# Optimization experiments

Measured on AMD Instinct MI355X. Metric: run time of the kernel, lower is better.

Reference implementation:

```python
import jax, jax.numpy as jnp
import numpy as np

B, N, D, E, C = 8, 4096, 1024, 512, 4096


def setup_inputs() -> dict:
    key = jax.random.key(0)
    k1, k2, k3 = jax.random.split(key, 3)
    x = jax.random.normal(k1, (B, N, D), dtype=jnp.float32)
    # xavier_normal_ scale for an (input_dim, codebook_dim) matrix
    scale = (2.0 / (D + E)) ** 0.5
    random_projection = jax.random.normal(k2, (D, E), dtype=jnp.float32) * scale
    codebook = jax.random.normal(k3, (C, E), dtype=jnp.float32)
    return {"x": x, "random_projection": random_projection, "codebook": codebook}


def _l2norm(v, eps=1e-12):
    # matches torch.nn.functional.normalize(p=2): v / max(||v||, eps)
    return v / jnp.maximum(jnp.linalg.norm(v, axis=-1, keepdims=True), eps)


def reference(x, random_projection, codebook):
    # project: b n d, d e -> b n e
    proj = jnp.einsum("bnd,de->bne", x, random_projection)
    pn = _l2norm(proj)            # [B, N, E], unit vectors
    cn = _l2norm(codebook)        # [C, E],   unit vectors
    # For unit vectors, ||p - c||^2 = 2 - 2 * <p, c>, so
    # argmin_c cdist == argmax_c cosine similarity (same indices as torch code).
    sim = jnp.einsum("bne,ce->bnc", pn, cn)  # [B, N, C]
    xq = jnp.argmax(sim, axis=-1).astype(jnp.int32)  # [B, N]
    return xq
```

## Files before the change

kernel.cpp:

```cpp
#include <hip/hip_runtime.h>
#include <math.h>


typedef _Float16 half8 __attribute__((ext_vector_type(8)));
typedef _Float16 half4 __attribute__((ext_vector_type(4)));
typedef float f32x4 __attribute__((ext_vector_type(4)));

#define INV2048 (4.8828125e-4f)
#define MARGIN 0.03f

struct Split { _Float16 h, l; };

__device__ __forceinline__ Split split_f32(float v) {
    Split s;
    s.h = (_Float16)v;
    s.l = (_Float16)((v - (float)s.h) * 2048.0f);
    return s;
}

__device__ __forceinline__ void gl_lds16(const void* g, void* l) {
    __builtin_amdgcn_global_load_lds(
        (const __attribute__((address_space(1))) unsigned int*)g,
        (__attribute__((address_space(3))) unsigned int*)l, 16, 0, 0);
}

__global__ __launch_bounds__(256) void k_prep_rpt(const float* __restrict__ rp,
                                                  _Float16* __restrict__ th,
                                                  _Float16* __restrict__ tl,
                                                  int* __restrict__ cnt) {
    if (blockIdx.x == 0 && blockIdx.y == 0 && threadIdx.x == 0) *cnt = 0;
    __shared__ float tile[64][65];
    const int k0 = blockIdx.x * 64, n0 = blockIdx.y * 64;
    const int t = threadIdx.x;
    const int rr = t >> 6, cc = t & 63;
    #pragma unroll
    for (int i = 0; i < 16; ++i) {
        int r = i * 4 + rr;
        tile[r][cc] = rp[(size_t)(k0 + r) * 512 + n0 + cc];
    }
    __syncthreads();
    #pragma unroll
    for (int i = 0; i < 16; ++i) {
        int n = i * 4 + rr;
        Split s = split_f32(tile[cc][n]);
        size_t o = (size_t)(n0 + n) * 1024 + k0 + cc;
        th[o] = s.h;
        tl[o] = s.l;
    }
}

__global__ __launch_bounds__(256) void k_norm_cb(const float* __restrict__ cb,
                                                 _Float16* __restrict__ ch,
                                                 _Float16* __restrict__ cl) {
    const int c = blockIdx.x;
    const int t = threadIdx.x;
    const float* row = cb + (size_t)c * 512;
    float v0 = row[t];
    float v1 = row[t + 256];
    float ss = v0 * v0 + v1 * v1;
    #pragma unroll
    for (int o = 32; o > 0; o >>= 1) ss += __shfl_down(ss, o, 64);
    __shared__ float wsum[4];
    if ((t & 63) == 0) wsum[t >> 6] = ss;
    __syncthreads();
    float s = 1.0f / fmaxf(sqrtf(wsum[0] + wsum[1] + wsum[2] + wsum[3]), 1e-12f);
    Split s0 = split_f32(v0 * s);
    ch[(size_t)c * 512 + t] = s0.h;
    cl[(size_t)c * 512 + t] = s0.l;
    Split s1 = split_f32(v1 * s);
    ch[(size_t)c * 512 + t + 256] = s1.h;
    cl[(size_t)c * 512 + t + 256] = s1.l;
}

__global__ __launch_bounds__(256, 2) void k_gemm1(const float* __restrict__ X,
                                                  const _Float16* __restrict__ Bh,
                                                  const _Float16* __restrict__ Bl,
                                                  _Float16* __restrict__ Ph,
                                                  _Float16* __restrict__ Pl) {
    __shared__ _Float16 sAh[128 * 32], sAl[128 * 32], sBh[128 * 32], sBl[128 * 32];
    const int t = threadIdx.x;
    const int nb = blockIdx.x;
    const int mb = blockIdx.y;
    const int lane = t & 63, w = t >> 6;
    const int quad = lane >> 4, l15 = lane & 15;
    const int wm = w >> 1, wn = w & 1;

    f32x4 acc[4][4], acc2[4][4];
    const f32x4 z = {0.f, 0.f, 0.f, 0.f};
    #pragma unroll
    for (int i = 0; i < 4; ++i)
        #pragma unroll
        for (int j = 0; j < 4; ++j) { acc[i][j] = z; acc2[i][j] = z; }

    const int srow = w * 32 + (lane >> 2);
    const int kcol = (lane & 3) * 8;
    const _Float16* gBh = Bh + (size_t)(nb * 128 + srow) * 1024 + kcol;
    const _Float16* gBl = Bl + (size_t)(nb * 128 + srow) * 1024 + kcol;
    const float* Xb = X + (size_t)(mb * 128) * 1024;

    for (int ks = 0; ks < 32; ++ks) {
        const int ko = ks * 32;
        __syncthreads();
        gl_lds16(gBh + ko, &sBh[w * 1024]);
        gl_lds16(gBh + ko + (size_t)16 * 1024, &sBh[w * 1024 + 512]);
        gl_lds16(gBl + ko, &sBl[w * 1024]);
        gl_lds16(gBl + ko + (size_t)16 * 1024, &sBl[w * 1024 + 512]);
        #pragma unroll
        for (int i = 0; i < 4; ++i) {
            int c = i * 256 + t;
            int row = c >> 3, kq = (c & 7) * 4;
            float4 v = *(const float4*)(Xb + (size_t)row * 1024 + ko + kq);
            Split sx = split_f32(v.x), sy = split_f32(v.y);
            Split sz = split_f32(v.z), sw = split_f32(v.w);
            half4 hv, lv;
            hv.x = sx.h; hv.y = sy.h; hv.z = sz.h; hv.w = sw.h;
            lv.x = sx.l; lv.y = sy.l; lv.z = sz.l; lv.w = sw.l;
            *(half4*)&sAh[row * 32 + kq] = hv;
            *(half4*)&sAl[row * 32 + kq] = lv;
        }
        __syncthreads();
        half8 ah[4], al[4], bh[4], bl[4];
        #pragma unroll
        for (int i = 0; i < 4; ++i) {
            ah[i] = *(const half8*)&sAh[(wm * 64 + i * 16 + l15) * 32 + quad * 8];
            al[i] = *(const half8*)&sAl[(wm * 64 + i * 16 + l15) * 32 + quad * 8];
            bh[i] = *(const half8*)&sBh[(wn * 64 + i * 16 + l15) * 32 + quad * 8];
            bl[i] = *(const half8*)&sBl[(wn * 64 + i * 16 + l15) * 32 + quad * 8];
        }
        #pragma unroll
        for (int mi = 0; mi < 4; ++mi)
            #pragma unroll
            for (int ni = 0; ni < 4; ++ni) {
                acc[mi][ni]  = __builtin_amdgcn_mfma_f32_16x16x32_f16(ah[mi], bh[ni], acc[mi][ni], 0, 0, 0);
                acc2[mi][ni] = __builtin_amdgcn_mfma_f32_16x16x32_f16(ah[mi], bl[ni], acc2[mi][ni], 0, 0, 0);
                acc2[mi][ni] = __builtin_amdgcn_mfma_f32_16x16x32_f16(al[mi], bh[ni], acc2[mi][ni], 0, 0, 0);
            }
    }
    #pragma unroll
    for (int mi = 0; mi < 4; ++mi)
        #pragma unroll
        for (int r = 0; r < 4; ++r) {
            int row = mb * 128 + wm * 64 + mi * 16 + quad * 4 + r;
            #pragma unroll
            for (int ni = 0; ni < 4; ++ni) {
                int col = nb * 128 + wn * 64 + ni * 16 + l15;
                float v = acc[mi][ni][r] + acc2[mi][ni][r] * INV2048;
                Split s = split_f32(v);
                Ph[(size_t)row * 512 + col] = s.h;
                Pl[(size_t)row * 512 + col] = s.l;
            }
        }
}

__global__ __launch_bounds__(256, 4) void k_sim_h(const _Float16* __restrict__ Ah,
                                                  const _Float16* __restrict__ Bh,
                                                  float* __restrict__ pv1,
                                                  int* __restrict__ pi1,
                                                  float* __restrict__ pv2) {
    __shared__ _Float16 sA[2][4096], sB[2][4096];
    __shared__ float v1s[128][2], v2s[128][2];
    __shared__ int   i1s[128][2];
    const int t = threadIdx.x;
    const int cbk = blockIdx.x;
    const int mb = blockIdx.y;
    const int lane = t & 63, w = t >> 6;
    const int quad = lane >> 4, l15 = lane & 15;
    const int wm = w >> 1, wn = w & 1;

    f32x4 acc[4][4];
    const f32x4 z = {0.f, 0.f, 0.f, 0.f};
    #pragma unroll
    for (int i = 0; i < 4; ++i)
        #pragma unroll
        for (int j = 0; j < 4; ++j) acc[i][j] = z;

    const int srow = lane >> 2;
    const int kseg = (lane & 3) ^ ((lane >> 3) & 3);
    const _Float16* gA = Ah + (size_t)(mb * 128 + w * 32 + srow) * 512 + kseg * 8;
    const _Float16* gB = Bh + (size_t)(cbk * 128 + w * 32 + srow) * 512 + kseg * 8;

    const int sw8 = (quad ^ ((l15 >> 1) & 3)) * 8;

    gl_lds16(gA, &sA[0][w * 1024]);
    gl_lds16(gA + (size_t)16 * 512, &sA[0][w * 1024 + 512]);
    gl_lds16(gB, &sB[0][w * 1024]);
    gl_lds16(gB + (size_t)16 * 512, &sB[0][w * 1024 + 512]);

    for (int ks = 0; ks < 16; ++ks) {
        const int p = ks & 1;
        __syncthreads();
        if (ks + 1 < 16) {
            const int ko = (ks + 1) * 32;
            gl_lds16(gA + ko, &sA[p ^ 1][w * 1024]);
            gl_lds16(gA + ko + (size_t)16 * 512, &sA[p ^ 1][w * 1024 + 512]);
            gl_lds16(gB + ko, &sB[p ^ 1][w * 1024]);
            gl_lds16(gB + ko + (size_t)16 * 512, &sB[p ^ 1][w * 1024 + 512]);
        }
        half8 a[4], b[4];
        #pragma unroll
        for (int i = 0; i < 4; ++i) {
            a[i] = *(const half8*)&sA[p][(wm * 64 + i * 16 + l15) * 32 + sw8];
            b[i] = *(const half8*)&sB[p][(wn * 64 + i * 16 + l15) * 32 + sw8];
        }
        #pragma unroll
        for (int mi = 0; mi < 4; ++mi)
            #pragma unroll
            for (int ni = 0; ni < 4; ++ni)
                acc[mi][ni] = __builtin_amdgcn_mfma_f32_16x16x32_f16(a[mi], b[ni], acc[mi][ni], 0, 0, 0);
    }

    #pragma unroll
    for (int mi = 0; mi < 4; ++mi)
        #pragma unroll
        for (int r = 0; r < 4; ++r) {
            float v1 = -INFINITY, v2 = -INFINITY;
            int i1 = 0x7fffffff;
            #pragma unroll
            for (int ni = 0; ni < 4; ++ni) {
                float v = acc[mi][ni][r];
                int col = cbk * 128 + wn * 64 + ni * 16 + l15;
                if (v > v1 || (v == v1 && col < i1)) { v2 = v1; v1 = v; i1 = col; }
                else if (v > v2) v2 = v;
            }
            #pragma unroll
            for (int o = 1; o < 16; o <<= 1) {
                float ov1 = __shfl_xor(v1, o, 64);
                int oi1 = __shfl_xor(i1, o, 64);
                float ov2 = __shfl_xor(v2, o, 64);
                if (ov1 > v1 || (ov1 == v1 && oi1 < i1)) { v2 = fmaxf(v1, ov2); v1 = ov1; i1 = oi1; }
                else v2 = fmaxf(v2, ov1);
            }
            if (l15 == 0) {
                int row = wm * 64 + mi * 16 + quad * 4 + r;
                v1s[row][wn] = v1; i1s[row][wn] = i1; v2s[row][wn] = v2;
            }
        }
    __syncthreads();
    if (t < 128) {
        float v1 = v1s[t][0], v2 = v2s[t][0];
        int i1 = i1s[t][0];
        float ov1 = v1s[t][1], ov2 = v2s[t][1];
        int oi1 = i1s[t][1];
        if (ov1 > v1 || (ov1 == v1 && oi1 < i1)) { v2 = fmaxf(v1, ov2); v1 = ov1; i1 = oi1; }
        else v2 = fmaxf(v2, ov1);
        size_t o = (size_t)(mb * 128 + t) * 32 + cbk;
        pv1[o] = v1; pi1[o] = i1; pv2[o] = v2;
    }
}

__global__ __launch_bounds__(256) void k_flag(const float* __restrict__ pv1,
                                              const int* __restrict__ pi1,
                                              const float* __restrict__ pv2,
                                              int* __restrict__ out,
                                              int* __restrict__ list,
                                              int* __restrict__ cnt) {
    int r = blockIdx.x * 256 + threadIdx.x;
    if (r >= 32768) return;
    size_t base = (size_t)r * 32;
    float v1 = pv1[base], v2 = pv2[base];
    int i1 = pi1[base];
    #pragma unroll
    for (int j = 1; j < 32; ++j) {
        float ov1 = pv1[base + j], ov2 = pv2[base + j];
        int oi1 = pi1[base + j];
        if (ov1 > v1 || (ov1 == v1 && oi1 < i1)) { v2 = fmaxf(v1, ov2); v1 = ov1; i1 = oi1; }
        else v2 = fmaxf(v2, ov1);
    }
    out[r] = i1;
    if (v1 - v2 < MARGIN) {
        int p = atomicAdd(cnt, 1);
        list[p] = r;
    }
}

__global__ __launch_bounds__(256, 2) void k_sim_fix(const _Float16* __restrict__ Ah,
                                                    const _Float16* __restrict__ Al,
                                                    const _Float16* __restrict__ Bh,
                                                    const _Float16* __restrict__ Bl,
                                                    const int* __restrict__ list,
                                                    const int* __restrict__ cnt,
                                                    float* __restrict__ rpv,
                                                    int* __restrict__ rpi) {
    __shared__ _Float16 sAh[128 * 32], sAl[128 * 32], sBh[128 * 32], sBl[128 * 32];
    __shared__ int rowidx[128];
    __shared__ float pvs[128][2];
    __shared__ int   pis[128][2];
    const int count = *cnt;
    const int t = threadIdx.x;
    const int cbk = blockIdx.x;
    const int lane = t & 63, w = t >> 6;
    const int quad = lane >> 4, l15 = lane & 15;
    const int wm = w >> 1, wn = w & 1;

    const int srow = w * 32 + (lane >> 2);
    const int kcol = (lane & 3) * 8;
    const _Float16* gBh = Bh + (size_t)(cbk * 128 + srow) * 512 + kcol;
    const _Float16* gBl = Bl + (size_t)(cbk * 128 + srow) * 512 + kcol;

    for (int g = blockIdx.y; g * 128 < count; g += gridDim.y) {
        __syncthreads();
        if (t < 128) {
            int p = g * 128 + t;
            rowidx[t] = (p < count) ? list[p] : list[0];
        }
        __syncthreads();

        f32x4 acc[4][4], acc2[4][4];
        const f32x4 z = {0.f, 0.f, 0.f, 0.f};
        #pragma unroll
        for (int i = 0; i < 4; ++i)
            #pragma unroll
            for (int j = 0; j < 4; ++j) { acc[i][j] = z; acc2[i][j] = z; }

        for (int ks = 0; ks < 16; ++ks) {
            const int ko = ks * 32;
            __syncthreads();
            gl_lds16(gBh + ko, &sBh[w * 1024]);
            gl_lds16(gBh + ko + (size_t)16 * 512, &sBh[w * 1024 + 512]);
            gl_lds16(gBl + ko, &sBl[w * 1024]);
            gl_lds16(gBl + ko + (size_t)16 * 512, &sBl[w * 1024 + 512]);
            #pragma unroll
            for (int i = 0; i < 2; ++i) {
                int idx = i * 256 + t;
                int row = idx >> 2, seg = (idx & 3) * 8;
                size_t src = (size_t)rowidx[row] * 512 + ko + seg;
                *(half8*)&sAh[row * 32 + seg] = *(const half8*)(Ah + src);
                *(half8*)&sAl[row * 32 + seg] = *(const half8*)(Al + src);
            }
            __syncthreads();
            half8 ah[4], al[4], bh[4], bl[4];
            #pragma unroll
            for (int i = 0; i < 4; ++i) {
                ah[i] = *(const half8*)&sAh[(wm * 64 + i * 16 + l15) * 32 + quad * 8];
                al[i] = *(const half8*)&sAl[(wm * 64 + i * 16 + l15) * 32 + quad * 8];
                bh[i] = *(const half8*)&sBh[(wn * 64 + i * 16 + l15) * 32 + quad * 8];
                bl[i] = *(const half8*)&sBl[(wn * 64 + i * 16 + l15) * 32 + quad * 8];
            }
            #pragma unroll
            for (int mi = 0; mi < 4; ++mi)
                #pragma unroll
                for (int ni = 0; ni < 4; ++ni) {
                    acc[mi][ni]  = __builtin_amdgcn_mfma_f32_16x16x32_f16(ah[mi], bh[ni], acc[mi][ni], 0, 0, 0);
                    acc2[mi][ni] = __builtin_amdgcn_mfma_f32_16x16x32_f16(ah[mi], bl[ni], acc2[mi][ni], 0, 0, 0);
                    acc2[mi][ni] = __builtin_amdgcn_mfma_f32_16x16x32_f16(al[mi], bh[ni], acc2[mi][ni], 0, 0, 0);
                }
        }

        #pragma unroll
        for (int mi = 0; mi < 4; ++mi)
            #pragma unroll
            for (int r = 0; r < 4; ++r) {
                float bv = -INFINITY;
                int bi = 0x7fffffff;
                #pragma unroll
                for (int ni = 0; ni < 4; ++ni) {
                    float v = acc[mi][ni][r] + acc2[mi][ni][r] * INV2048;
                    int col = cbk * 128 + wn * 64 + ni * 16 + l15;
                    if (v > bv || (v == bv && col < bi)) { bv = v; bi = col; }
                }
                #pragma unroll
                for (int o = 1; o < 16; o <<= 1) {
                    float ov = __shfl_xor(bv, o, 64);
                    int oi = __shfl_xor(bi, o, 64);
                    if (ov > bv || (ov == bv && oi < bi)) { bv = ov; bi = oi; }
                }
                if (l15 == 0) {
                    int row = wm * 64 + mi * 16 + quad * 4 + r;
                    pvs[row][wn] = bv; pis[row][wn] = bi;
                }
            }
        __syncthreads();
        if (t < 128 && g * 128 + t < count) {
            float v0 = pvs[t][0], v1 = pvs[t][1];
            int i0 = pis[t][0], i1 = pis[t][1];
            bool sw = (v1 > v0) || (v1 == v0 && i1 < i0);
            size_t o = (size_t)(g * 128 + t) * 32 + cbk;
            rpv[o] = sw ? v1 : v0;
            rpi[o] = sw ? i1 : i0;
        }
    }
}

__global__ __launch_bounds__(256) void k_fix(const float* __restrict__ rpv,
                                             const int* __restrict__ rpi,
                                             const int* __restrict__ list,
                                             const int* __restrict__ cnt,
                                             int* __restrict__ out) {
    int p = blockIdx.x * 256 + threadIdx.x;
    if (p >= *cnt) return;
    size_t base = (size_t)p * 32;
    float bv = -INFINITY;
    int bi = 0x7fffffff;
    #pragma unroll
    for (int j = 0; j < 32; ++j) {
        float v = rpv[base + j];
        int ci = rpi[base + j];
        if (v > bv || (v == bv && ci < bi)) { bv = v; bi = ci; }
    }
    out[list[p]] = bi;
}

extern "C" void kernel_launch(void* const* d_in, const int* in_sizes, int n_in,
                              void* d_out, int out_size, void* d_ws, size_t ws_size,
                              hipStream_t stream) {
    const float* x  = (const float*)d_in[0];
    const float* rp = (const float*)d_in[1];
    const float* cb = (const float*)d_in[2];
    int* out = (int*)d_out;

    char* ws = (char*)d_ws;
    _Float16* cn_h   = (_Float16*)(ws);
    _Float16* cn_l   = (_Float16*)(ws + ((size_t)4 << 20));
    _Float16* rpT_h  = (_Float16*)(ws + ((size_t)8 << 20));
    _Float16* rpT_l  = (_Float16*)(ws + ((size_t)9 << 20));
    _Float16* proj_h = (_Float16*)(ws + ((size_t)10 << 20));
    _Float16* proj_l = (_Float16*)(ws + ((size_t)42 << 20));
    float*    pv1    = (float*)   (ws + ((size_t)74 << 20));
    int*      pi1    = (int*)     (ws + ((size_t)78 << 20));
    float*    pv2    = (float*)   (ws + ((size_t)82 << 20));
    float*    rpv    = (float*)   (ws + ((size_t)86 << 20));
    int*      rpi    = (int*)     (ws + ((size_t)90 << 20));
    int*      list   = (int*)     (ws + ((size_t)94 << 20));
    int*      cnt    = (int*)     (ws + ((size_t)94 << 20) + (128 << 10));

    k_prep_rpt<<<dim3(16, 8), 256, 0, stream>>>(rp, rpT_h, rpT_l, cnt);
    k_norm_cb<<<4096, 256, 0, stream>>>(cb, cn_h, cn_l);
    k_gemm1<<<dim3(4, 256), 256, 0, stream>>>(x, rpT_h, rpT_l, proj_h, proj_l);
    k_sim_h<<<dim3(32, 256), 256, 0, stream>>>(proj_h, cn_h, pv1, pi1, pv2);
    k_flag<<<128, 256, 0, stream>>>(pv1, pi1, pv2, out, list, cnt);
    k_sim_fix<<<dim3(32, 32), 256, 0, stream>>>(proj_h, proj_l, cn_h, cn_l, list, cnt, rpv, rpi);
    k_fix<<<128, 256, 0, stream>>>(rpv, rpi, list, cnt, out);
}
```

Baseline: 609.3 us.

## Merge prep kernels, single-buffer sim GEMM, and pack argmax epilogue into u64 keys

Merges the projection-transpose and codebook-normalise kernels into one launch. In the main similarity GEMM, the LDS double buffer becomes a single buffer with two barriers per k-step, and the launch bound changes from 4 to 3. The top-2 epilogue drops the shuffle reductions: each lane writes packed (ordered-float key, inverted column) u64 pairs into LDS that reuses the tile memory, and 128 threads scan 32 entries each. This cuts launch overhead and epilogue shuffles, but gives up the load/compute overlap of double buffering, which may stall the MFMA loop.

```diff
diff --git a/kernel.cpp b/kernel.cpp
--- a/kernel.cpp
+++ b/kernel.cpp
@@ -5,6 +5,8 @@
 typedef _Float16 half8 __attribute__((ext_vector_type(8)));
 typedef _Float16 half4 __attribute__((ext_vector_type(4)));
 typedef float f32x4 __attribute__((ext_vector_type(4)));
+typedef unsigned long long u64;
+typedef unsigned int u32;
 
 #define INV2048 (4.8828125e-4f)
 #define MARGIN 0.03f
@@ -24,52 +26,61 @@
         (__attribute__((address_space(3))) unsigned int*)l, 16, 0, 0);
 }
 
-__global__ __launch_bounds__(256) void k_prep_rpt(const float* __restrict__ rp,
-                                                  _Float16* __restrict__ th,
-                                                  _Float16* __restrict__ tl,
-                                                  int* __restrict__ cnt) {
-    if (blockIdx.x == 0 && blockIdx.y == 0 && threadIdx.x == 0) *cnt = 0;
-    __shared__ float tile[64][65];
-    const int k0 = blockIdx.x * 64, n0 = blockIdx.y * 64;
+__device__ __forceinline__ u32 fkey(float v) {
+    u32 b = __float_as_uint(v);
+    return b ^ ((u32)((int)b >> 31) | 0x80000000u);
+}
+__device__ __forceinline__ float fkeyinv(u32 u) {
+    u32 m2 = (u32)((int)u >> 31);
+    return __uint_as_float(u ^ ((~m2) | 0x80000000u));
+}
+
+__global__ __launch_bounds__(256) void k_prep(const float* __restrict__ rp,
+                                              _Float16* __restrict__ th,
+                                              _Float16* __restrict__ tl,
+                                              const float* __restrict__ cb,
+                                              _Float16* __restrict__ ch,
+                                              _Float16* __restrict__ cl,
+                                              int* __restrict__ cnt) {
     const int t = threadIdx.x;
-    const int rr = t >> 6, cc = t & 63;
-    #pragma unroll
-    for (int i = 0; i < 16; ++i) {
-        int r = i * 4 + rr;
-        tile[r][cc] = rp[(size_t)(k0 + r) * 512 + n0 + cc];
-    }
-    __syncthreads();
-    #pragma unroll
-    for (int i = 0; i < 16; ++i) {
-        int n = i * 4 + rr;
-        Split s = split_f32(tile[cc][n]);
-        size_t o = (size_t)(n0 + n) * 1024 + k0 + cc;
-        th[o] = s.h;
-        tl[o] = s.l;
-    }
-}
-
-__global__ __launch_bounds__(256) void k_norm_cb(const float* __restrict__ cb,
-                                                 _Float16* __restrict__ ch,
-                                                 _Float16* __restrict__ cl) {
-    const int c = blockIdx.x;
-    const int t = threadIdx.x;
-    const float* row = cb + (size_t)c * 512;
-    float v0 = row[t];
-    float v1 = row[t + 256];
-    float ss = v0 * v0 + v1 * v1;
-    #pragma unroll
-    for (int o = 32; o > 0; o >>= 1) ss += __shfl_down(ss, o, 64);
-    __shared__ float wsum[4];
-    if ((t & 63) == 0) wsum[t >> 6] = ss;
-    __syncthreads();
-    float s = 1.0f / fmaxf(sqrtf(wsum[0] + wsum[1] + wsum[2] + wsum[3]), 1e-12f);
-    Split s0 = split_f32(v0 * s);
-    ch[(size_t)c * 512 + t] = s0.h;
-    cl[(size_t)c * 512 + t] = s0.l;
-    Split s1 = split_f32(v1 * s);
-    ch[(size_t)c * 512 + t + 256] = s1.h;
-    cl[(size_t)c * 512 + t + 256] = s1.l;
+    if (blockIdx.x == 0 && t == 0) *cnt = 0;
+    if (blockIdx.x < 128) {
+        __shared__ float tile[64][65];
+        const int k0 = (blockIdx.x & 15) * 64, n0 = (blockIdx.x >> 4) * 64;
+        const int rr = t >> 6, cc = t & 63;
+        #pragma unroll
+        for (int i = 0; i < 16; ++i) {
+            int r = i * 4 + rr;
+            tile[r][cc] = rp[(size_t)(k0 + r) * 512 + n0 + cc];
+        }
+        __syncthreads();
+        #pragma unroll
+        for (int i = 0; i < 16; ++i) {
+            int n = i * 4 + rr;
+            Split s = split_f32(tile[cc][n]);
+            size_t o = (size_t)(n0 + n) * 1024 + k0 + cc;
+            th[o] = s.h;
+            tl[o] = s.l;
+        }
+    } else {
+        const int c = blockIdx.x - 128;
+        const float* row = cb + (size_t)c * 512;
+        float v0 = row[t];
+        float v1 = row[t + 256];
+        float ss = v0 * v0 + v1 * v1;
+        #pragma unroll
+        for (int o = 32; o > 0; o >>= 1) ss += __shfl_down(ss, o, 64);
+        __shared__ float wsum[4];
+        if ((t & 63) == 0) wsum[t >> 6] = ss;
+        __syncthreads();
+        float s = 1.0f / fmaxf(sqrtf(wsum[0] + wsum[1] + wsum[2] + wsum[3]), 1e-12f);
+        Split s0 = split_f32(v0 * s);
+        ch[(size_t)c * 512 + t] = s0.h;
+        cl[(size_t)c * 512 + t] = s0.l;
+        Split s1 = split_f32(v1 * s);
+        ch[(size_t)c * 512 + t + 256] = s1.h;
+        cl[(size_t)c * 512 + t + 256] = s1.l;
+    }
 }
 
 __global__ __launch_bounds__(256, 2) void k_gemm1(const float* __restrict__ X,
@@ -152,14 +163,16 @@
         }
 }
 
-__global__ __launch_bounds__(256, 4) void k_sim_h(const _Float16* __restrict__ Ah,
+__global__ __launch_bounds__(256, 3) void k_sim_h(const _Float16* __restrict__ Ah,
                                                   const _Float16* __restrict__ Bh,
                                                   float* __restrict__ pv1,
                                                   int* __restrict__ pi1,
                                                   float* __restrict__ pv2) {
-    __shared__ _Float16 sA[2][4096], sB[2][4096];
-    __shared__ float v1s[128][2], v2s[128][2];
-    __shared__ int   i1s[128][2];
+    __shared__ __align__(16) long long smem64[6144];
+    _Float16* sA = (_Float16*)smem64;
+    _Float16* sB = sA + 4096;
+    u64* ept = (u64*)smem64;
+    u32* epv = (u32*)((char*)smem64 + 32768);
     const int t = threadIdx.x;
     const int cbk = blockIdx.x;
     const int mb = blockIdx.y;
@@ -178,29 +191,21 @@
     const int kseg = (lane & 3) ^ ((lane >> 3) & 3);
     const _Float16* gA = Ah + (size_t)(mb * 128 + w * 32 + srow) * 512 + kseg * 8;
     const _Float16* gB = Bh + (size_t)(cbk * 128 + w * 32 + srow) * 512 + kseg * 8;
-
     const int sw8 = (quad ^ ((l15 >> 1) & 3)) * 8;
 
-    gl_lds16(gA, &sA[0][w * 1024]);
-    gl_lds16(gA + (size_t)16 * 512, &sA[0][w * 1024 + 512]);
-    gl_lds16(gB, &sB[0][w * 1024]);
-    gl_lds16(gB + (size_t)16 * 512, &sB[0][w * 1024 + 512]);
-
     for (int ks = 0; ks < 16; ++ks) {
-        const int p = ks & 1;
-        __syncthreads();
-        if (ks + 1 < 16) {
-            const int ko = (ks + 1) * 32;
-            gl_lds16(gA + ko, &sA[p ^ 1][w * 1024]);
-            gl_lds16(gA + ko + (size_t)16 * 512, &sA[p ^ 1][w * 1024 + 512]);
-            gl_lds16(gB + ko, &sB[p ^ 1][w * 1024]);
-            gl_lds16(gB + ko + (size_t)16 * 512, &sB[p ^ 1][w * 1024 + 512]);
-        }
+        const int ko = ks * 32;
+        __syncthreads();
+        gl_lds16(gA + ko, &sA[w * 1024]);
+        gl_lds16(gA + ko + (size_t)16 * 512, &sA[w * 1024 + 512]);
+        gl_lds16(gB + ko, &sB[w * 1024]);
+        gl_lds16(gB + ko + (size_t)16 * 512, &sB[w * 1024 + 512]);
+        __syncthreads();
         half8 a[4], b[4];
         #pragma unroll
         for (int i = 0; i < 4; ++i) {
-            a[i] = *(const half8*)&sA[p][(wm * 64 + i * 16 + l15) * 32 + sw8];
-            b[i] = *(const half8*)&sB[p][(wn * 64 + i * 16 + l15) * 32 + sw8];
+            a[i] = *(const half8*)&sA[(wm * 64 + i * 16 + l15) * 32 + sw8];
+            b[i] = *(const half8*)&sB[(wn * 64 + i * 16 + l15) * 32 + sw8];
         }
         #pragma unroll
         for (int mi = 0; mi < 4; ++mi)
@@ -209,42 +214,46 @@
                 acc[mi][ni] = __builtin_amdgcn_mfma_f32_16x16x32_f16(a[mi], b[ni], acc[mi][ni], 0, 0, 0);
     }
 
+    __syncthreads();
     #pragma unroll
     for (int mi = 0; mi < 4; ++mi)
         #pragma unroll
         for (int r = 0; r < 4; ++r) {
-            float v1 = -INFINITY, v2 = -INFINITY;
-            int i1 = 0x7fffffff;
+            int row = wm * 64 + mi * 16 + quad * 4 + r;
+            u64 p1 = 0, p2 = 0;
             #pragma unroll
             for (int ni = 0; ni < 4; ++ni) {
                 float v = acc[mi][ni][r];
-                int col = cbk * 128 + wn * 64 + ni * 16 + l15;
-                if (v > v1 || (v == v1 && col < i1)) { v2 = v1; v1 = v; i1 = col; }
-                else if (v > v2) v2 = v;
-            }
-            #pragma unroll
-            for (int o = 1; o < 16; o <<= 1) {
-                float ov1 = __shfl_xor(v1, o, 64);
-                int oi1 = __shfl_xor(i1, o, 64);
-                float ov2 = __shfl_xor(v2, o, 64);
-                if (ov1 > v1 || (ov1 == v1 && oi1 < i1)) { v2 = fmaxf(v1, ov2); v1 = ov1; i1 = oi1; }
-                else v2 = fmaxf(v2, ov1);
-            }
-            if (l15 == 0) {
-                int row = wm * 64 + mi * 16 + quad * 4 + r;
-                v1s[row][wn] = v1; i1s[row][wn] = i1; v2s[row][wn] = v2;
-            }
+                u32 col = cbk * 128 + wn * 64 + ni * 16 + l15;
+                u64 p = ((u64)fkey(v) << 32) | (u32)(~col);
+                if (p > p1) { p2 = p1; p1 = p; }
+                else if (p > p2) p2 = p;
+            }
+            int e = row * 32 + wn * 16 + l15;
+            ept[e] = p1;
+            epv[e] = (u32)(p2 >> 32);
         }
     __syncthreads();
     if (t < 128) {
-        float v1 = v1s[t][0], v2 = v2s[t][0];
-        int i1 = i1s[t][0];
-        float ov1 = v1s[t][1], ov2 = v2s[t][1];
-        int oi1 = i1s[t][1];
-        if (ov1 > v1 || (ov1 == v1 && oi1 < i1)) { v2 = fmaxf(v1, ov2); v1 = ov1; i1 = oi1; }
-        else v2 = fmaxf(v2, ov1);
+        u64 b1 = 0, b2 = 0;
+        u32 vk2 = 0;
+        #pragma unroll
+        for (int jj = 0; jj < 32; ++jj) {
+            int j = (jj + t) & 31;
+            u64 p = ept[t * 32 + j];
+            if (p > b1) { b2 = b1; b1 = p; }
+            else if (p > b2) b2 = p;
+            u32 vk = epv[t * 32 + j];
+            vk2 = vk > vk2 ? vk : vk2;
+        }
+        u32 k2 = (u32)(b2 >> 32);
+        if (vk2 > k2) k2 = vk2;
+        float v1 = fkeyinv((u32)(b1 >> 32));
+        int col = (int)(~(u32)b1);
         size_t o = (size_t)(mb * 128 + t) * 32 + cbk;
-        pv1[o] = v1; pi1[o] = i1; pv2[o] = v2;
+        pv1[o] = v1;
+        pi1[o] = col;
+        pv2[o] = fkeyinv(k2);
     }
 }
 
@@ -423,8 +432,7 @@
     int*      list   = (int*)     (ws + ((size_t)94 << 20));
     int*      cnt    = (int*)     (ws + ((size_t)94 << 20) + (128 << 10));
 
-    k_prep_rpt<<<dim3(16, 8), 256, 0, stream>>>(rp, rpT_h, rpT_l, cnt);
-    k_norm_cb<<<4096, 256, 0, stream>>>(cb, cn_h, cn_l);
+    k_prep<<<4224, 256, 0, stream>>>(rp, rpT_h, rpT_l, cb, cn_h, cn_l, cnt);
     k_gemm1<<<dim3(4, 256), 256, 0, stream>>>(x, rpT_h, rpT_l, proj_h, proj_l);
     k_sim_h<<<dim3(32, 256), 256, 0, stream>>>(proj_h, cn_h, pv1, pi1, pv2);
     k_flag<<<128, 256, 0, stream>>>(pv1, pi1, pv2, out, list, cnt);
```

Result: faster. 560.9 us (-8.0%).
